# Kernel tuning notes

Hardware: AMD Instinct MI355X
Metric: run time of the kernel (lower is better)

The kernel has to match this reference:

```python
import jax, jax.numpy as jnp
import numpy as np

EPS = 1e-5
NUM_HEADS = 8


def _conv(x, w, pad, dil=1, groups=1, b=None):
    y = jax.lax.conv_general_dilated(
        x, w, (1, 1), pad, rhs_dilation=(dil, dil),
        dimension_numbers=('NCHW', 'OIHW', 'NCHW'), feature_group_count=groups)
    if b is not None:
        y = y + b[None, :, None, None]
    return y


def _bn_relu(x, gamma, beta):
    # BatchNorm2d in training mode: batch statistics over (N,H,W) per channel
    mu = x.mean(axis=(0, 2, 3), keepdims=True)
    var = x.var(axis=(0, 2, 3), keepdims=True)
    y = (x - mu) / jnp.sqrt(var + EPS) * gamma[None, :, None, None] + beta[None, :, None, None]
    return jax.nn.relu(y)


def _ln(x, w, b):
    # WithBias LayerNorm over channel dim (to_3d makes C the last axis)
    mu = x.mean(axis=1, keepdims=True)
    var = x.var(axis=1, keepdims=True)
    return (x - mu) / jnp.sqrt(var + EPS) * w[None, :, None, None] + b[None, :, None, None]


def _l2n(t):
    # torch F.normalize: x / max(||x||_2, 1e-12)
    return t / jnp.maximum(jnp.linalg.norm(t, axis=-1, keepdims=True), 1e-12)


def _forward(x, ln_w, ln_b, wd1, gd1, bd1, wd2, gd2, bd2, wd3, gd3, bd3,
             w_out1, w1, b1, w2, b2, w3, b3, w4, b4, w5, b5, w6, b6, w_out2):
    B, C, H, W = x.shape
    head, ch = NUM_HEADS, C // NUM_HEADS
    x1 = _ln(x, ln_w, ln_b)
    # dilated dense-conv branch (DConv2d = conv -> BN -> ReLU), dilations [1,6,12]
    x11 = _bn_relu(_conv(x, wd1, ((0, 0), (0, 0))), gd1, bd1)
    x12 = _bn_relu(_conv(x, wd2, ((6, 6), (6, 6)), dil=6), gd2, bd2)
    x13 = _bn_relu(_conv(x, wd3, ((12, 12), (12, 12)), dil=12), gd3, bd3)
    out2 = _conv(x11 + x12 + x13, w_out1, ((0, 0), (0, 0))) + x
    # six depthwise conv branches, summed
    att = (_conv(x1, w1, ((0, 0), (2, 2)), groups=C, b=b1)
           + _conv(x1, w2, ((2, 2), (0, 0)), groups=C, b=b2)
           + _conv(x1, w3, ((0, 0), (0, 0)), groups=C, b=b3)
           + _conv(x1, w4, ((1, 1), (1, 1)), groups=C, b=b4)
           + _conv(x1, w5, ((0, 0), (3, 3)), groups=C, b=b5)
           + _conv(x1, w6, ((3, 3), (0, 0)), groups=C, b=b6))
    out1 = _conv(att, w_out2, ((0, 0), (0, 0)))

    def r_hwc(t):  # b (head c) h w -> b head h (w c)
        return t.reshape(B, head, ch, H, W).transpose(0, 1, 3, 4, 2).reshape(B, head, H, W * ch)

    def r_whc(t):  # b (head c) h w -> b head w (h c)
        return t.reshape(B, head, ch, H, W).transpose(0, 1, 4, 3, 2).reshape(B, head, W, H * ch)

    k1 = _l2n(r_hwc(out1))
    v1 = r_hwc(out1)
    k2 = _l2n(r_whc(out2))
    v2 = r_whc(out2)
    q2 = _l2n(r_whc(out1))
    q1 = _l2n(r_whc(out2))
    A1 = jax.nn.softmax(q1 @ jnp.swapaxes(k1, -2, -1), axis=-1)  # [B,head,W,H]
    out3 = A1 @ v1 + q1
    A2 = jax.nn.softmax(q2 @ jnp.swapaxes(k2, -2, -1), axis=-1)
    out4 = A2 @ v2 + q2
    # b head h (w c) -> b (head c) h w
    o3 = out3.reshape(B, head, H, W, ch).transpose(0, 1, 4, 2, 3).reshape(B, C, H, W)
    # b head w (h c) -> b (head c) h w
    o4 = out4.reshape(B, head, W, H, ch).transpose(0, 1, 4, 3, 2).reshape(B, C, H, W)
    return _conv(o3, w_out2, ((0, 0), (0, 0))) + _conv(o4, w_out2, ((0, 0), (0, 0))) + x


def setup_inputs() -> dict:
    key = jax.random.key(0)
    ks = jax.random.split(key, 16)
    B, C, H, W = 8, 128, 128, 128

    def rn(k, shape, s):
        return jax.random.normal(k, shape, jnp.float32) * s

    inp = {}
    inp['x'] = jax.random.normal(ks[0], (B, C, H, W), jnp.float32)
    inp['ln_w'] = jnp.ones((C,), jnp.float32)
    inp['ln_b'] = jnp.zeros((C,), jnp.float32)
    inp['wd1'] = rn(ks[1], (C, C, 1, 1), 0.1)
    inp['gd1'] = jnp.ones((C,), jnp.float32)
    inp['bd1'] = jnp.zeros((C,), jnp.float32)
    inp['wd2'] = rn(ks[2], (C, C, 3, 3), 0.04)
    inp['gd2'] = jnp.ones((C,), jnp.float32)
    inp['bd2'] = jnp.zeros((C,), jnp.float32)
    inp['wd3'] = rn(ks[3], (C, C, 3, 3), 0.04)
    inp['gd3'] = jnp.ones((C,), jnp.float32)
    inp['bd3'] = jnp.zeros((C,), jnp.float32)
    inp['w_out1'] = rn(ks[4], (C, C, 1, 1), 0.09)
    inp['w1'] = rn(ks[5], (C, 1, 1, 5), 0.3)
    inp['b1'] = jnp.zeros((C,), jnp.float32)
    inp['w2'] = rn(ks[6], (C, 1, 5, 1), 0.3)
    inp['b2'] = jnp.zeros((C,), jnp.float32)
    inp['w3'] = rn(ks[7], (C, 1, 1, 1), 0.5)
    inp['b3'] = jnp.zeros((C,), jnp.float32)
    inp['w4'] = rn(ks[8], (C, 1, 3, 3), 0.2)
    inp['b4'] = jnp.zeros((C,), jnp.float32)
    inp['w5'] = rn(ks[9], (C, 1, 1, 7), 0.25)
    inp['b5'] = jnp.zeros((C,), jnp.float32)
    inp['w6'] = rn(ks[10], (C, 1, 7, 1), 0.25)
    inp['b6'] = jnp.zeros((C,), jnp.float32)
    inp['w_out2'] = rn(ks[11], (C, C, 1, 1), 0.09)
    return inp


def reference(x, ln_w, ln_b, wd1, gd1, bd1, wd2, gd2, bd2, wd3, gd3, bd3,
              w_out1, w1, b1, w2, b2, w3, b3, w4, b4, w5, b5, w6, b6, w_out2):
    return _forward(x, ln_w, ln_b, wd1, gd1, bd1, wd2, gd2, bd2, wd3, gd3, bd3,
                    w_out1, w1, b1, w2, b2, w3, b3, w4, b4, w5, b5, w6, b6, w_out2)
```

## Files before the change

kernel.cpp:

```cpp
#include <hip/hip_runtime.h>

#define Bb 8
#define Cc 128
#define Hh 128
#define Ww 128
#define HW 16384
#define CHW (Cc*HW)
#define NHW (Bb*HW)
#define CH 16
#define EPS 1e-5f
#define NSLICE 16

typedef __attribute__((ext_vector_type(8))) short bf16x8;
typedef __attribute__((ext_vector_type(4))) float f32x4;

static __device__ __forceinline__ short f2b(float f) {
  unsigned u = __float_as_uint(f);
  unsigned lsb = (u >> 16) & 1;
  return (short)((u + 0x7fffu + lsb) >> 16);
}
static __device__ __forceinline__ float b2f(short s) {
  return __uint_as_float(((unsigned)(unsigned short)s) << 16);
}

static __device__ __forceinline__ void stats_epilogue(
    float* __restrict__ statp, f32x4 acc[4][4], int co0, int quad, int lm)
{
  statp += (blockIdx.x & (NSLICE-1)) * 768;
  #pragma unroll
  for (int i = 0; i < 4; ++i) {
    f32x4 s = acc[i][0] + acc[i][1] + acc[i][2] + acc[i][3];
    f32x4 q = acc[i][0]*acc[i][0] + acc[i][1]*acc[i][1]
            + acc[i][2]*acc[i][2] + acc[i][3]*acc[i][3];
    #pragma unroll
    for (int m = 1; m < 16; m <<= 1) {
      #pragma unroll
      for (int e = 0; e < 4; ++e) {
        s[e] += __shfl_xor(s[e], m);
        q[e] += __shfl_xor(q[e], m);
      }
    }
    if (lm == 0) {
      int co = co0 + i*16 + quad*4;
      #pragma unroll
      for (int e = 0; e < 4; ++e) {
        atomicAdd(&statp[co + e], s[e]);
        atomicAdd(&statp[128 + co + e], q[e]);
      }
    }
  }
}

__global__ __launch_bounds__(256) void k_ln(const float* __restrict__ x,
    const float* __restrict__ g, const float* __restrict__ be,
    float* __restrict__ y)
{
  int p = blockIdx.x*256 + threadIdx.x;
  int b = p >> 14, hw = p & 16383;
  const float* xp = x + (long)b*CHW + hw;
  float s = 0.f, q = 0.f;
  for (int c = 0; c < Cc; ++c) { float v = xp[c*HW]; s += v; q += v*v; }
  float mu = s * (1.f/Cc);
  float var = q * (1.f/Cc) - mu*mu;
  float rstd = rsqrtf(var + EPS);
  float* yp = y + (long)b*CHW + hw;
  for (int c = 0; c < Cc; ++c) {
    float v = xp[c*HW];
    yp[c*HW] = (v - mu) * rstd * g[c] + be[c];
  }
}

__global__ __launch_bounds__(256) void k_reorg3b(const float* __restrict__ Wt, short* __restrict__ out)
{
  int idx = blockIdx.x*256 + threadIdx.x;
  int tap = idx >> 14, r = idx & 16383;
  out[idx] = f2b(Wt[r*9 + tap]);
}

__global__ __launch_bounds__(256) void k_cast(const float* __restrict__ in, short* __restrict__ out)
{
  int i = blockIdx.x*256 + threadIdx.x;
  out[i] = f2b(in[i]);
}

__global__ __launch_bounds__(256) void k_zero(float* p, int n)
{
  int i = blockIdx.x*256 + threadIdx.x;
  if (i < n) p[i] = 0.f;
}

__global__ __launch_bounds__(256) void k_nhwc(const float* __restrict__ in, short* __restrict__ out)
{
  __shared__ float Ls[32][33];
  int bid = blockIdx.x;
  int hwt = bid & 511, c4 = (bid>>9)&3, b = bid>>11;
  int hw0 = hwt << 5, c0 = c4 << 5;
  int t = threadIdx.x;
  int hl = t & 31, cl = t >> 5;
  const float* p = in + (long)b*CHW + hw0;
  for (int r = cl; r < 32; r += 8)
    Ls[r][hl] = p[(long)(c0+r)*HW + hl];
  __syncthreads();
  short* q = out + ((long)b*HW + hw0)*Cc + c0;
  int ccl = t & 31, hl0 = t >> 5;
  for (int r = hl0; r < 32; r += 8)
    q[(long)r*Cc + ccl] = f2b(Ls[ccl][r]);
}

__global__ __launch_bounds__(256) void k_nhwcb(const short* __restrict__ in, short* __restrict__ out)
{
  __shared__ short Ls[32][34];
  int bid = blockIdx.x;
  int hwt = bid & 511, c4 = (bid>>9)&3, b = bid>>11;
  int hw0 = hwt << 5, c0 = c4 << 5;
  int t = threadIdx.x;
  int hl = t & 31, cl = t >> 5;
  const short* p = in + (long)b*CHW + hw0;
  for (int r = cl; r < 32; r += 8)
    Ls[r][hl] = p[(long)(c0+r)*HW + hl];
  __syncthreads();
  short* q = out + ((long)b*HW + hw0)*Cc + c0;
  int ccl = t & 31, hl0 = t >> 5;
  for (int r = hl0; r < 32; r += 8)
    q[(long)r*Cc + ccl] = Ls[ccl][r];
}

__global__ __launch_bounds__(256,2) void k_mconv(const short* __restrict__ X,
    const short* __restrict__ W, float* __restrict__ Y, int k3, int dil,
    float* __restrict__ statp)
{
  __shared__ short Ws[128*136];
  __shared__ short Xs[152*136];
  int b = blockIdx.x >> 7, h = blockIdx.x & 127;
  int t = threadIdx.x;
  int wave = t >> 6, lane = t & 63;
  int co0 = (wave >> 1) << 6, sp0 = (wave & 1) << 6;
  int lm = lane & 15, quad = lane >> 4;
  f32x4 acc[4][4];
  #pragma unroll
  for (int i = 0; i < 4; ++i)
    #pragma unroll
    for (int j = 0; j < 4; ++j) acc[i][j] = (f32x4){0.f,0.f,0.f,0.f};
  int half = k3 >> 1;

  {
    f32x4 z = {0.f,0.f,0.f,0.f};
    for (int i = t; i < 408; i += 256) {
      int r = i / 17, o = i - r*17;
      int row = r < 12 ? r : r + 128;
      *(f32x4*)(Xs + row*136 + o*8) = z;
    }
  }

  for (int kh = 0; kh < k3; ++kh) {
    int hs = h + (kh - half)*dil;
    if ((unsigned)hs >= (unsigned)Hh) continue;
    __syncthreads();
    {
      const short* xr = X + ((long)(b*Hh + hs)*Ww)*Cc;
      #pragma unroll
      for (int it = 0; it < 8; ++it) {
        int i = t + it*256;
        int row = i >> 4, off = (i & 15) << 3;
        *(f32x4*)(Xs + (12 + row)*136 + off) = *(const f32x4*)(xr + (long)row*Cc + off);
      }
    }
    for (int kw = 0; kw < k3; ++kw) {
      int dw = (kw - half)*dil;
      if (kw) __syncthreads();
      {
        const short* wt = W + (kh*k3 + kw)*16384;
        #pragma unroll
        for (int it = 0; it < 8; ++it) {
          int i = t + it*256;
          int row = i >> 4, off = (i & 15) << 3;
          *(f32x4*)(Ws + row*136 + off) = *(const f32x4*)(wt + (long)row*128 + off);
        }
      }
      __syncthreads();
      int xrow0 = 12 + dw + sp0;
      for (int kc = 0; kc < 4; ++kc) {
        int k0 = kc << 5;
        bf16x8 af[4], bfr[4];
        #pragma unroll
        for (int i = 0; i < 4; ++i)
          af[i] = *(const bf16x8*)(Ws + (co0 + i*16 + lm)*136 + k0 + quad*8);
        #pragma unroll
        for (int j = 0; j < 4; ++j)
          bfr[j] = *(const bf16x8*)(Xs + (xrow0 + j*16 + lm)*136 + k0 + quad*8);
        #pragma unroll
        for (int i = 0; i < 4; ++i)
          #pragma unroll
          for (int j = 0; j < 4; ++j)
            acc[i][j] = __builtin_amdgcn_mfma_f32_16x16x32_bf16(af[i], bfr[j], acc[i][j], 0, 0, 0);
      }
    }
  }
  float* yb = Y + ((long)(b*Hh + h)*Ww)*Cc;
  #pragma unroll
  for (int i = 0; i < 4; ++i) {
    int co = co0 + i*16 + quad*4;
    #pragma unroll
    for (int j = 0; j < 4; ++j) {
      int wc = sp0 + j*16 + lm;
      *(f32x4*)(yb + (long)wc*Cc + co) = acc[i][j];
    }
  }
  if (statp) stats_epilogue(statp, acc, co0, quad, lm);
}

__global__ __launch_bounds__(256,4) void k_mconv1(const short* __restrict__ X,
    const short* __restrict__ W, const float* __restrict__ res,
    float* __restrict__ Y, int nhwc, float* __restrict__ statp)
{
  __shared__ short Ws[128*136];
  int b = blockIdx.x >> 7, h = blockIdx.x & 127;
  int t = threadIdx.x;
  int wave = t >> 6, lane = t & 63;
  int co0 = (wave >> 1) << 6, sp0 = (wave & 1) << 6;
  int lm = lane & 15, quad = lane >> 4;
  #pragma unroll
  for (int it = 0; it < 8; ++it) {
    int i = t + it*256;
    int row = i >> 4, off = (i & 15) << 3;
    *(f32x4*)(Ws + row*136 + off) = *(const f32x4*)(W + (long)row*128 + off);
  }
  f32x4 acc[4][4];
  #pragma unroll
  for (int i = 0; i < 4; ++i)
    #pragma unroll
    for (int j = 0; j < 4; ++j) acc[i][j] = (f32x4){0.f,0.f,0.f,0.f};
  const short* xr = X + ((long)(b*Hh + h)*Ww)*Cc;
  __syncthreads();
  #pragma unroll
  for (int kc = 0; kc < 4; ++kc) {
    int k0 = kc << 5;
    bf16x8 af[4], bfr[4];
    #pragma unroll
    for (int j = 0; j < 4; ++j)
      bfr[j] = *(const bf16x8*)(xr + (long)(sp0 + j*16 + lm)*Cc + k0 + quad*8);
    #pragma unroll
    for (int i = 0; i < 4; ++i)
      af[i] = *(const bf16x8*)(Ws + (co0 + i*16 + lm)*136 + k0 + quad*8);
    #pragma unroll
    for (int i = 0; i < 4; ++i)
      #pragma unroll
      for (int j = 0; j < 4; ++j)
        acc[i][j] = __builtin_amdgcn_mfma_f32_16x16x32_bf16(af[i], bfr[j], acc[i][j], 0, 0, 0);
  }
  if (nhwc) {
    float* yb = Y + ((long)(b*Hh + h)*Ww)*Cc;
    #pragma unroll
    for (int i = 0; i < 4; ++i) {
      int co = co0 + i*16 + quad*4;
      #pragma unroll
      for (int j = 0; j < 4; ++j) {
        int wc = sp0 + j*16 + lm;
        *(f32x4*)(yb + (long)wc*Cc + co) = acc[i][j];
      }
    }
    if (statp) stats_epilogue(statp, acc, co0, quad, lm);
  } else {
    __syncthreads();
    float* scr = (float*)Ws + wave*320;
    int co_l = lane >> 2, wq = (lane & 3) << 2;
    #pragma unroll
    for (int i = 0; i < 4; ++i) {
      #pragma unroll
      for (int j = 0; j < 4; ++j) {
        #pragma unroll
        for (int r = 0; r < 4; ++r)
          scr[(quad*4 + r)*20 + lm] = acc[i][j][r];
        f32x4 vv = *(f32x4*)(scr + co_l*20 + wq);
        int co = co0 + i*16 + co_l;
        int wc = sp0 + j*16 + wq;
        long idx = ((long)(b*Cc + co)*Hh + h)*Ww + wc;
        if (res) vv += *(const f32x4*)(res + idx);
        *(f32x4*)(Y + idx) = vv;
      }
    }
  }
}

__global__ __launch_bounds__(128) void k_bnfin(const float* __restrict__ stats,
    const float* __restrict__ g1, const float* __restrict__ be1,
    const float* __restrict__ g2, const float* __restrict__ be2,
    const float* __restrict__ g3, const float* __restrict__ be3,
    float* __restrict__ so)
{
  int c = threadIdx.x;
  const float inv = 1.f/(float)NHW;
  const float* gs[3] = {g1, g2, g3};
  const float* bs[3] = {be1, be2, be3};
  #pragma unroll
  for (int tsel = 0; tsel < 3; ++tsel) {
    float su = 0.f, qu = 0.f;
    for (int sl = 0; sl < NSLICE; ++sl) {
      su += stats[sl*768 + tsel*256 + c];
      qu += stats[sl*768 + tsel*256 + 128 + c];
    }
    float mu = su*inv;
    float var = qu*inv - mu*mu;
    float s = rsqrtf(var + EPS)*gs[tsel][c];
    so[tsel*256 + c] = s;
    so[tsel*256 + 128 + c] = bs[tsel][c] - mu*s;
  }
}

__global__ __launch_bounds__(256) void k_bnapply(const float* __restrict__ y1,
    const float* __restrict__ y2, const float* __restrict__ y3,
    const float* __restrict__ so, short* __restrict__ sb)
{
  long e = ((long)blockIdx.x*256 + threadIdx.x) * 8;
  int c = (int)(e & 127);
  f32x4 s1a = *(const f32x4*)(so + c),        s1b = *(const f32x4*)(so + c + 4);
  f32x4 o1a = *(const f32x4*)(so + 128 + c),  o1b = *(const f32x4*)(so + 132 + c);
  f32x4 s2a = *(const f32x4*)(so + 256 + c),  s2b = *(const f32x4*)(so + 260 + c);
  f32x4 o2a = *(const f32x4*)(so + 384 + c),  o2b = *(const f32x4*)(so + 388 + c);
  f32x4 s3a = *(const f32x4*)(so + 512 + c),  s3b = *(const f32x4*)(so + 516 + c);
  f32x4 o3a = *(const f32x4*)(so + 640 + c),  o3b = *(const f32x4*)(so + 644 + c);
  f32x4 v1a = *(const f32x4*)(y1 + e), v1b = *(const f32x4*)(y1 + e + 4);
  f32x4 v2a = *(const f32x4*)(y2 + e), v2b = *(const f32x4*)(y2 + e + 4);
  f32x4 v3a = *(const f32x4*)(y3 + e), v3b = *(const f32x4*)(y3 + e + 4);
  float r[8];
  #pragma unroll
  for (int k = 0; k < 4; ++k) {
    r[k] = fmaxf(fmaf(v1a[k], s1a[k], o1a[k]), 0.f)
         + fmaxf(fmaf(v2a[k], s2a[k], o2a[k]), 0.f)
         + fmaxf(fmaf(v3a[k], s3a[k], o3a[k]), 0.f);
    r[4+k] = fmaxf(fmaf(v1b[k], s1b[k], o1b[k]), 0.f)
           + fmaxf(fmaf(v2b[k], s2b[k], o2b[k]), 0.f)
           + fmaxf(fmaf(v3b[k], s3b[k], o3b[k]), 0.f);
  }
  int4 o;
  o.x = ((int)(unsigned short)f2b(r[1])<<16) | (unsigned short)f2b(r[0]);
  o.y = ((int)(unsigned short)f2b(r[3])<<16) | (unsigned short)f2b(r[2]);
  o.z = ((int)(unsigned short)f2b(r[5])<<16) | (unsigned short)f2b(r[4]);
  o.w = ((int)(unsigned short)f2b(r[7])<<16) | (unsigned short)f2b(r[6]);
  *(int4*)(sb + e) = o;
}

__global__ __launch_bounds__(256) void k_dw2(const float* __restrict__ X,
    const float* __restrict__ w1, const float* __restrict__ b1,
    const float* __restrict__ w2, const float* __restrict__ b2,
    const float* __restrict__ w3, const float* __restrict__ b3,
    const float* __restrict__ w4, const float* __restrict__ b4,
    const float* __restrict__ w5, const float* __restrict__ b5,
    const float* __restrict__ w6, const float* __restrict__ b6,
    short* __restrict__ Y)
{
  __shared__ float Ls[38][136];
  int bid = blockIdx.x;
  int tile = bid & 3, plane = bid >> 2;
  int c = plane & 127;
  int h0 = tile << 5;
  int t = threadIdx.x;

  float hcoef[7], vcoef[7], k9[9];
  #pragma unroll
  for (int d = 0; d < 7; ++d) { hcoef[d] = w5[c*7+d]; vcoef[d] = w6[c*7+d]; }
  #pragma unroll
  for (int d = 1; d < 6; ++d) { hcoef[d] += w1[c*5+d-1]; vcoef[d] += w2[c*5+d-1]; }
  hcoef[3] += w3[c];
  #pragma unroll
  for (int k = 0; k < 9; ++k) k9[k] = w4[c*9+k];
  float bias = b1[c]+b2[c]+b3[c]+b4[c]+b5[c]+b6[c];

  const float* xp = X + (long)plane*HW;

  f32x4* lz = (f32x4*)&Ls[0][0];
  for (int i = t; i < 1292; i += 256) lz[i] = (f32x4){0.f,0.f,0.f,0.f};
  __syncthreads();
  for (int i = t; i < 1216; i += 256) {
    int r = i >> 5, cg = (i & 31) << 2;
    int h = h0 - 3 + r;
    if ((unsigned)h < 128u)
      *(f32x4*)&Ls[r][4 + cg] = *(const f32x4*)(xp + h*128 + cg);
  }
  __syncthreads();

  int g = t & 31, rs = t >> 5;
  int w0 = g << 2;
  short* Yp = Y + (long)plane*HW;

  for (int ro = 0; ro < 4; ++ro) {
    int lr = rs + (ro << 3);
    int R = lr + 3;
    f32x4 a0 = *(const f32x4*)&Ls[R][w0];
    f32x4 a1 = *(const f32x4*)&Ls[R][w0+4];
    f32x4 a2 = *(const f32x4*)&Ls[R][w0+8];
    f32x4 u0 = *(const f32x4*)&Ls[R-1][w0];
    f32x4 u1 = *(const f32x4*)&Ls[R-1][w0+4];
    f32x4 u2 = *(const f32x4*)&Ls[R-1][w0+8];
    f32x4 d0 = *(const f32x4*)&Ls[R+1][w0];
    f32x4 d1 = *(const f32x4*)&Ls[R+1][w0+4];
    f32x4 d2 = *(const f32x4*)&Ls[R+1][w0+8];
    f32x4 v3u = *(const f32x4*)&Ls[R-3][w0+4];
    f32x4 v2u = *(const f32x4*)&Ls[R-2][w0+4];
    f32x4 v2d = *(const f32x4*)&Ls[R+2][w0+4];
    f32x4 v3d = *(const f32x4*)&Ls[R+3][w0+4];

    float cr[12], ur[12], dr[12];
    #pragma unroll
    for (int k = 0; k < 4; ++k) {
      cr[k] = a0[k]; cr[4+k] = a1[k]; cr[8+k] = a2[k];
      ur[k] = u0[k]; ur[4+k] = u1[k]; ur[8+k] = u2[k];
      dr[k] = d0[k]; dr[4+k] = d1[k]; dr[8+k] = d2[k];
    }

    float o[4];
    #pragma unroll
    for (int j = 0; j < 4; ++j) {
      float acc = bias;
      #pragma unroll
      for (int d = 0; d < 7; ++d) acc = fmaf(hcoef[d], cr[j+d+1], acc);
      acc = fmaf(vcoef[0], v3u[j], acc);
      acc = fmaf(vcoef[1], v2u[j], acc);
      acc = fmaf(vcoef[2], ur[j+4], acc);
      acc = fmaf(vcoef[3], cr[j+4], acc);
      acc = fmaf(vcoef[4], dr[j+4], acc);
      acc = fmaf(vcoef[5], v2d[j], acc);
      acc = fmaf(vcoef[6], v3d[j], acc);
      #pragma unroll
      for (int kw = 0; kw < 3; ++kw) {
        acc = fmaf(k9[kw],   ur[j+3+kw], acc);
        acc = fmaf(k9[3+kw], cr[j+3+kw], acc);
        acc = fmaf(k9[6+kw], dr[j+3+kw], acc);
      }
      o[j] = acc;
    }
    int2 ov;
    ov.x = ((int)(unsigned short)f2b(o[1])<<16) | (unsigned short)f2b(o[0]);
    ov.y = ((int)(unsigned short)f2b(o[3])<<16) | (unsigned short)f2b(o[2]);
    *(int2*)(Yp + (h0 + lr)*128 + w0) = ov;
  }
}

__global__ __launch_bounds__(256) void k_normh(const float* __restrict__ out1, float* __restrict__ invn)
{
  __shared__ float red[256];
  int bid = blockIdx.x;
  int h = bid & 127; int bh = bid >> 7;
  int b = bh >> 3, hd = bh & 7;
  const float* p = out1 + ((long)(b*Cc + hd*CH)*Hh + h)*Ww;
  float s = 0.f;
  for (int e = threadIdx.x; e < 2048; e += 256) {
    int c = e >> 7, w = e & 127;
    float v = p[(long)c*HW + w];
    s += v*v;
  }
  red[threadIdx.x] = s; __syncthreads();
  for (int st = 128; st > 0; st >>= 1) {
    if (threadIdx.x < st) red[threadIdx.x] += red[threadIdx.x+st];
    __syncthreads();
  }
  if (threadIdx.x == 0) invn[bid] = 1.f/fmaxf(sqrtf(red[0]), 1e-12f);
}

__global__ __launch_bounds__(256) void k_normw_part(const float* __restrict__ out1,
    const float* __restrict__ out2, float* __restrict__ acc1, float* __restrict__ acc2)
{
  __shared__ float red[4][256];
  int bid = blockIdx.x;
  int c = bid & 15, bh = (bid >> 4) & 63, tsel = bid >> 10;
  int b = bh >> 3, hd = bh & 7;
  const float* p = (tsel ? out2 : out1) + (long)(b*Cc + hd*CH + c)*HW;
  int t = threadIdx.x;
  const float4* p4 = (const float4*)p;
  float s0 = 0.f, s1 = 0.f, s2 = 0.f, s3 = 0.f;
  for (int i = t; i < 4096; i += 256) {
    float4 v = p4[i];
    s0 += v.x*v.x; s1 += v.y*v.y; s2 += v.z*v.z; s3 += v.w*v.w;
  }
  red[0][t] = s0; red[1][t] = s1; red[2][t] = s2; red[3][t] = s3;
  __syncthreads();
  if (t < 128) {
    int j = t >> 5;
    int g = t & 31;
    float tot = 0.f;
    #pragma unroll
    for (int r = 0; r < 8; ++r) tot += red[j][g + r*32];
    atomicAdd((tsel ? acc2 : acc1) + bh*128 + g*4 + j, tot);
  }
}

__global__ __launch_bounds__(256) void k_finw(float* __restrict__ p)
{
  int i = blockIdx.x*256 + threadIdx.x;
  float v = p[i];
  p[i] = 1.f/fmaxf(sqrtf(v), 1e-12f);
}

__global__ __launch_bounds__(256) void k_thx(const float* __restrict__ out1,
    const float* __restrict__ out2,
    short* __restrict__ out1T, short* __restrict__ out2T,
    short* __restrict__ out1H, short* __restrict__ out2H)
{
  __shared__ float Ls[32][33];
  int bid = blockIdx.x;
  int wt = bid&3, ht=(bid>>2)&3, c=(bid>>4)&127, b=(bid>>11)&7, src=bid>>14;
  const float* in = (src ? out2 : out1) + (long)(b*128+c)*16384;
  long tbase = ((long)(b*8 + (c>>4))*128)*2048 + (c&15)*128;
  short* pT = (src ? out2T : out1T) + tbase;
  short* pH; long hstr;
  if (src) { pH = out2H + (long)(b*128+c)*16384; hstr = 128; }
  else     { pH = out1H + tbase;                 hstr = 2048; }
  int h0 = ht*32, w0 = wt*32;
  int t = threadIdx.x, li = t&31, r0 = t>>5;
  for (int r = r0; r < 32; r += 8)
    Ls[r][li] = in[(h0+r)*128 + w0 + li];
  __syncthreads();
  for (int r = r0; r < 32; r += 8) {
    pT[(long)(w0+r)*2048 + h0 + li] = f2b(Ls[li][r]);
    pH[(long)(h0+r)*hstr + w0 + li] = f2b(Ls[r][li]);
  }
}

__global__ __launch_bounds__(256) void k_attnS_m(
    const short* __restrict__ out1T, const short* __restrict__ out2T,
    const short* __restrict__ out1H,
    const float* __restrict__ invn1h, const float* __restrict__ invn1w,
    const float* __restrict__ invn2w,
    short* __restrict__ A1b, short* __restrict__ A2b)
{
  __shared__ short As[128*72];
  __shared__ short Bs[128*72];
  int bid = blockIdx.x;
  int type = bid >> 6, bh = bid & 63;
  const short* Aop = (type ? out1T : out2T) + (long)bh*262144;
  const short* Bop = (type ? out2T : out1H) + (long)bh*262144;
  const float* invrow = (type ? invn1w : invn2w) + bh*128;
  const float* invcol = (type ? invn2w : invn1h) + bh*128;
  short* Aout = (type ? A2b : A1b) + (long)bh*16384;
  int t = threadIdx.x;
  int wave = t >> 6, lane = t & 63, lm = lane & 15, quad = lane >> 4;
  int m0 = wave << 5;
  f32x4 acc[2][8];
  #pragma unroll
  for (int i = 0; i < 2; ++i)
    #pragma unroll
    for (int j = 0; j < 8; ++j) acc[i][j] = (f32x4){0.f,0.f,0.f,0.f};
  for (int kc = 0; kc < 32; ++kc) {
    int k0 = kc << 6;
    __syncthreads();
    #pragma unroll
    for (int i = 0; i < 4; ++i) {
      int e = t + i*256;
      int row = e >> 3, off = (e & 7) << 3;
      *(float4*)(As + row*72 + off) = *(const float4*)(Aop + (long)row*2048 + k0 + off);
      *(float4*)(Bs + row*72 + off) = *(const float4*)(Bop + (long)row*2048 + k0 + off);
    }
    __syncthreads();
    #pragma unroll
    for (int ks = 0; ks < 64; ks += 32) {
      bf16x8 af[2], bfj[8];
      #pragma unroll
      for (int i = 0; i < 2; ++i)
        af[i] = *(const bf16x8*)(As + (m0 + i*16 + lm)*72 + ks + quad*8);
      #pragma unroll
      for (int j = 0; j < 8; ++j)
        bfj[j] = *(const bf16x8*)(Bs + (j*16 + lm)*72 + ks + quad*8);
      #pragma unroll
      for (int i = 0; i < 2; ++i)
        #pragma unroll
        for (int j = 0; j < 8; ++j)
          acc[i][j] = __builtin_amdgcn_mfma_f32_16x16x32_bf16(af[i], bfj[j], acc[i][j], 0, 0, 0);
    }
  }
  float colv[8];
  #pragma unroll
  for (int j = 0; j < 8; ++j) colv[j] = invcol[j*16 + lm];
  #pragma unroll
  for (int i = 0; i < 2; ++i) {
    #pragma unroll
    for (int r = 0; r < 4; ++r) {
      int row = m0 + i*16 + quad*4 + r;
      float rs = invrow[row];
      float sv[8];
      float mx = -1e30f;
      #pragma unroll
      for (int j = 0; j < 8; ++j) {
        sv[j] = acc[i][j][r] * rs * colv[j];
        mx = fmaxf(mx, sv[j]);
      }
      mx = fmaxf(mx, __shfl_xor(mx, 1));
      mx = fmaxf(mx, __shfl_xor(mx, 2));
      mx = fmaxf(mx, __shfl_xor(mx, 4));
      mx = fmaxf(mx, __shfl_xor(mx, 8));
      float sum = 0.f;
      #pragma unroll
      for (int j = 0; j < 8; ++j) { sv[j] = __expf(sv[j] - mx); sum += sv[j]; }
      sum += __shfl_xor(sum, 1);
      sum += __shfl_xor(sum, 2);
      sum += __shfl_xor(sum, 4);
      sum += __shfl_xor(sum, 8);
      float inv = 1.f/sum;
      #pragma unroll
      for (int j = 0; j < 8; ++j)
        Aout[row*128 + j*16 + lm] = f2b(sv[j]*inv);
    }
  }
}

__global__ __launch_bounds__(256) void k_o34f(
    const short* __restrict__ A1b, const short* __restrict__ out1T,
    const short* __restrict__ out1H, const float* __restrict__ invn1w,
    const short* __restrict__ out2H, const short* __restrict__ A2b,
    const float* __restrict__ out2, const float* __restrict__ invn2w,
    short* __restrict__ o34b)
{
  __shared__ short As[128*72];
  __shared__ short Bs[128*72];
  int bid = blockIdx.x;
  int cf = bid & 127, b = bid >> 7;
  int hd = cf >> 4, c = cf & 15;
  int bh = b*8 + hd;
  const short* A0 = A1b + (long)bh*16384;
  const short* B0 = out1T + (long)bh*262144 + c*128;
  const short* A1_ = out2H + (long)(b*128 + cf)*16384;
  const short* B1_ = A2b + (long)bh*16384;
  const short* R = out1H + (long)bh*262144 + c*128;
  const float* o2p = out2 + (long)(b*128 + cf)*16384;
  const float* inw1 = invn1w + bh*128;
  const float* inw2 = invn2w + bh*128;
  short* O = o34b + (long)(b*128 + cf)*16384;
  int t = threadIdx.x;
  int wave = t >> 6, lane = t & 63, lm = lane & 15, quad = lane >> 4;
  int m0 = (wave >> 1) << 6, n0 = (wave & 1) << 6;
  f32x4 acc[4][4];
  #pragma unroll
  for (int i = 0; i < 4; ++i)
    #pragma unroll
    for (int j = 0; j < 4; ++j) acc[i][j] = (f32x4){0.f,0.f,0.f,0.f};
  for (int g = 0; g < 4; ++g) {
    const short* Asrc = (g < 2) ? A0 : A1_;
    const short* Bsrc = (g < 2) ? B0 : B1_;
    long Bst = (g < 2) ? 2048 : 128;
    int k0 = (g & 1) << 6;
    __syncthreads();
    #pragma unroll
    for (int i = 0; i < 4; ++i) {
      int e = t + i*256;
      int row = e >> 3, off = (e & 7) << 3;
      *(float4*)(As + row*72 + off) = *(const float4*)(Asrc + (long)row*128 + k0 + off);
      *(float4*)(Bs + row*72 + off) = *(const float4*)(Bsrc + (long)row*Bst + k0 + off);
    }
    __syncthreads();
    #pragma unroll
    for (int ks = 0; ks < 64; ks += 32) {
      bf16x8 af[4], bfj[4];
      #pragma unroll
      for (int i = 0; i < 4; ++i)
        af[i] = *(const bf16x8*)(As + (m0 + i*16 + lm)*72 + ks + quad*8);
      #pragma unroll
      for (int j = 0; j < 4; ++j)
        bfj[j] = *(const bf16x8*)(Bs + (n0 + j*16 + lm)*72 + ks + quad*8);
      #pragma unroll
      for (int i = 0; i < 4; ++i)
        #pragma unroll
        for (int j = 0; j < 4; ++j)
          acc[i][j] = __builtin_amdgcn_mfma_f32_16x16x32_bf16(af[i], bfj[j], acc[i][j], 0, 0, 0);
    }
  }
  float inwv[4];
  #pragma unroll
  for (int j = 0; j < 4; ++j) inwv[j] = inw1[n0 + j*16 + lm];
  #pragma unroll
  for (int i = 0; i < 4; ++i) {
    int row0 = m0 + i*16 + quad*4;
    f32x4 iv2 = *(const f32x4*)(inw2 + row0);
    #pragma unroll
    for (int j = 0; j < 4; ++j) {
      int col = n0 + j*16 + lm;
      f32x4 vq = *(const f32x4*)(o2p + (long)col*128 + row0);
      #pragma unroll
      for (int r = 0; r < 4; ++r)
        acc[i][j][r] += b2f(R[(long)(row0 + r)*2048 + col]) * inwv[j]
                      + vq[r] * iv2[r];
    }
  }
  __syncthreads();
  float* scr = (float*)As + wave*320;
  int co_l = lane >> 2, wq = (lane & 3) << 2;
  #pragma unroll
  for (int i = 0; i < 4; ++i) {
    #pragma unroll
    for (int j = 0; j < 4; ++j) {
      #pragma unroll
      for (int r = 0; r < 4; ++r)
        scr[(quad*4 + r)*20 + lm] = acc[i][j][r];
      f32x4 vv = *(f32x4*)(scr + co_l*20 + wq);
      int2 ov;
      ov.x = ((int)(unsigned short)f2b(vv[1])<<16) | (unsigned short)f2b(vv[0]);
      ov.y = ((int)(unsigned short)f2b(vv[3])<<16) | (unsigned short)f2b(vv[2]);
      *(int2*)(O + (long)(m0 + i*16 + co_l)*128 + n0 + j*16 + wq) = ov;
    }
  }
}

extern "C" void kernel_launch(void* const* d_in, const int* in_sizes, int n_in,
                              void* d_out, int out_size, void* d_ws, size_t ws_size,
                              hipStream_t stream)
{
  const float* x    = (const float*)d_in[0];
  const float* ln_w = (const float*)d_in[1];
  const float* ln_b = (const float*)d_in[2];
  const float* wd1  = (const float*)d_in[3];
  const float* gd1  = (const float*)d_in[4];
  const float* bd1  = (const float*)d_in[5];
  const float* wd2  = (const float*)d_in[6];
  const float* gd2  = (const float*)d_in[7];
  const float* bd2  = (const float*)d_in[8];
  const float* wd3  = (const float*)d_in[9];
  const float* gd3  = (const float*)d_in[10];
  const float* bd3  = (const float*)d_in[11];
  const float* w_out1 = (const float*)d_in[12];
  const float* w1 = (const float*)d_in[13]; const float* b1 = (const float*)d_in[14];
  const float* w2 = (const float*)d_in[15]; const float* b2 = (const float*)d_in[16];
  const float* w3 = (const float*)d_in[17]; const float* b3 = (const float*)d_in[18];
  const float* w4 = (const float*)d_in[19]; const float* b4 = (const float*)d_in[20];
  const float* w5 = (const float*)d_in[21]; const float* b5 = (const float*)d_in[22];
  const float* w6 = (const float*)d_in[23]; const float* b6 = (const float*)d_in[24];
  const float* w_out2 = (const float*)d_in[25];
  float* out = (float*)d_out;

  const long SLAB = 16777216L;
  float* buf0 = (float*)d_ws;
  float* buf1 = buf0 + SLAB;
  float* buf2 = buf1 + SLAB;
  float* dbuf = out;
  float* stats = buf2 + SLAB;
  float* invn1h = stats + NSLICE*768;
  float* invn1w = invn1h + 8192;
  float* invn2w = invn1w + 8192;
  short* wb2  = (short*)(invn2w + 8192);
  short* wb3  = wb2 + 147456;
  short* wb1  = wb3 + 147456;
  short* wbo1 = wb1 + 16384;
  short* wbo2 = wbo1 + 16384;
  short* A1b  = wbo2 + 16384;
  short* A2b  = A1b + 1048576;
  float* bnso = (float*)(A2b + 1048576);

  short* xb = (short*)buf0;
  short* sb = (short*)buf0;
  short* attb = (short*)dbuf;
  short* ab = (short*)buf1;
  short* out1T = (short*)dbuf;
  short* out2T = out1T + 16777216;
  short* out1H = (short*)buf1;
  short* out2H = out1H + 16777216;
  short* o34b = (short*)buf0;
  short* ob = (short*)buf1;

  k_zero<<<48, 256, 0, stream>>>(stats, NSLICE*768);
  k_zero<<<64, 256, 0, stream>>>(invn1w, 16384);
  k_reorg3b<<<576, 256, 0, stream>>>(wd2, wb2);
  k_reorg3b<<<576, 256, 0, stream>>>(wd3, wb3);
  k_cast<<<64, 256, 0, stream>>>(wd1, wb1);
  k_cast<<<64, 256, 0, stream>>>(w_out1, wbo1);
  k_cast<<<64, 256, 0, stream>>>(w_out2, wbo2);

  k_nhwc<<<16384, 256, 0, stream>>>(x, xb);
  k_mconv1<<<1024, 256, 0, stream>>>(xb, wb1, nullptr, buf1, 1, stats);
  k_mconv<<<1024, 256, 0, stream>>>(xb, wb2, buf2, 3, 6, stats + 256);
  k_mconv<<<1024, 256, 0, stream>>>(xb, wb3, dbuf, 3, 12, stats + 512);
  k_bnfin<<<1, 128, 0, stream>>>(stats, gd1, bd1, gd2, bd2, gd3, bd3, bnso);
  k_bnapply<<<8192, 256, 0, stream>>>(buf1, buf2, dbuf, bnso, sb);
  k_mconv1<<<1024, 256, 0, stream>>>(sb, wbo1, x, buf2, 0, nullptr);
  k_ln<<<512, 256, 0, stream>>>(x, ln_w, ln_b, buf0);
  k_dw2<<<4096, 256, 0, stream>>>(buf0, w1,b1,w2,b2,w3,b3,w4,b4,w5,b5,w6,b6, attb);
  k_nhwcb<<<16384, 256, 0, stream>>>(attb, ab);
  k_mconv1<<<1024, 256, 0, stream>>>(ab, wbo2, nullptr, buf0, 0, nullptr);
  k_normh<<<8192, 256, 0, stream>>>(buf0, invn1h);
  k_normw_part<<<2048, 256, 0, stream>>>(buf0, buf2, invn1w, invn2w);
  k_finw<<<64, 256, 0, stream>>>(invn1w);
  k_thx<<<32768, 256, 0, stream>>>(buf0, buf2, out1T, out2T, out1H, out2H);
  k_attnS_m<<<128, 256, 0, stream>>>(out1T, out2T, out1H,
                                     invn1h, invn1w, invn2w, A1b, A2b);
  k_o34f<<<1024, 256, 0, stream>>>(A1b, out1T, out1H, invn1w,
                                   out2H, A2b, buf2, invn2w, o34b);
  k_nhwcb<<<16384, 256, 0, stream>>>(o34b, ob);
  k_mconv1<<<1024, 256, 0, stream>>>(ob, wbo2, x, out, 0, nullptr);
}
```

Before: 758.8 us.

## Fuse L2-norm reductions into transpose kernel and split attention-score rows across blocks

Removes the separate k_normh and k_normw_part passes by computing the per-row and per-column squared sums from the shared-memory tile inside k_thx, accumulated with atomics, so out1/out2 are not re-read for normalisation. A single k_finw then converts all three norm buffers. Separately, k_attnS_m splits each 128-row score matrix into two 64-row halves, doubling the grid from 128 to 256 blocks for better occupancy at the cost of loading the B operand twice. This relies on invn1h, invn1w and invn2w being contiguous, and it adds many atomics to k_thx.

Result: no change. 765.3 us (+0.9%).

```diff
diff --git a/kernel.cpp b/kernel.cpp
--- a/kernel.cpp
+++ b/kernel.cpp
@@ -436,54 +436,6 @@
   }
 }
 
-__global__ __launch_bounds__(256) void k_normh(const float* __restrict__ out1, float* __restrict__ invn)
-{
-  __shared__ float red[256];
-  int bid = blockIdx.x;
-  int h = bid & 127; int bh = bid >> 7;
-  int b = bh >> 3, hd = bh & 7;
-  const float* p = out1 + ((long)(b*Cc + hd*CH)*Hh + h)*Ww;
-  float s = 0.f;
-  for (int e = threadIdx.x; e < 2048; e += 256) {
-    int c = e >> 7, w = e & 127;
-    float v = p[(long)c*HW + w];
-    s += v*v;
-  }
-  red[threadIdx.x] = s; __syncthreads();
-  for (int st = 128; st > 0; st >>= 1) {
-    if (threadIdx.x < st) red[threadIdx.x] += red[threadIdx.x+st];
-    __syncthreads();
-  }
-  if (threadIdx.x == 0) invn[bid] = 1.f/fmaxf(sqrtf(red[0]), 1e-12f);
-}
-
-__global__ __launch_bounds__(256) void k_normw_part(const float* __restrict__ out1,
-    const float* __restrict__ out2, float* __restrict__ acc1, float* __restrict__ acc2)
-{
-  __shared__ float red[4][256];
-  int bid = blockIdx.x;
-  int c = bid & 15, bh = (bid >> 4) & 63, tsel = bid >> 10;
-  int b = bh >> 3, hd = bh & 7;
-  const float* p = (tsel ? out2 : out1) + (long)(b*Cc + hd*CH + c)*HW;
-  int t = threadIdx.x;
-  const float4* p4 = (const float4*)p;
-  float s0 = 0.f, s1 = 0.f, s2 = 0.f, s3 = 0.f;
-  for (int i = t; i < 4096; i += 256) {
-    float4 v = p4[i];
-    s0 += v.x*v.x; s1 += v.y*v.y; s2 += v.z*v.z; s3 += v.w*v.w;
-  }
-  red[0][t] = s0; red[1][t] = s1; red[2][t] = s2; red[3][t] = s3;
-  __syncthreads();
-  if (t < 128) {
-    int j = t >> 5;
-    int g = t & 31;
-    float tot = 0.f;
-    #pragma unroll
-    for (int r = 0; r < 8; ++r) tot += red[j][g + r*32];
-    atomicAdd((tsel ? acc2 : acc1) + bh*128 + g*4 + j, tot);
-  }
-}
-
 __global__ __launch_bounds__(256) void k_finw(float* __restrict__ p)
 {
   int i = blockIdx.x*256 + threadIdx.x;
@@ -494,7 +446,8 @@
 __global__ __launch_bounds__(256) void k_thx(const float* __restrict__ out1,
     const float* __restrict__ out2,
     short* __restrict__ out1T, short* __restrict__ out2T,
-    short* __restrict__ out1H, short* __restrict__ out2H)
+    short* __restrict__ out1H, short* __restrict__ out2H,
+    float* __restrict__ n1h, float* __restrict__ n1w, float* __restrict__ n2w)
 {
   __shared__ float Ls[32][33];
   int bid = blockIdx.x;
@@ -510,6 +463,19 @@
   for (int r = r0; r < 32; r += 8)
     Ls[r][li] = in[(h0+r)*128 + w0 + li];
   __syncthreads();
+  int bhbase = (b*8 + (c>>4))*128;
+  if (t < 32) {
+    if (!src) {
+      float s = 0.f;
+      for (int k = 0; k < 32; ++k) { float v = Ls[t][k]; s += v*v; }
+      atomicAdd(&n1h[bhbase + h0 + t], s);
+    }
+  } else if (t < 64) {
+    int w = t - 32;
+    float s = 0.f;
+    for (int k = 0; k < 32; ++k) { float v = Ls[k][w]; s += v*v; }
+    atomicAdd((src ? n2w : n1w) + bhbase + w0 + w, s);
+  }
   for (int r = r0; r < 32; r += 8) {
     pT[(long)(w0+r)*2048 + h0 + li] = f2b(Ls[li][r]);
     pH[(long)(h0+r)*hstr + w0 + li] = f2b(Ls[r][li]);
@@ -523,82 +489,78 @@
     const float* __restrict__ invn2w,
     short* __restrict__ A1b, short* __restrict__ A2b)
 {
-  __shared__ short As[128*72];
+  __shared__ short As[64*72];
   __shared__ short Bs[128*72];
   int bid = blockIdx.x;
-  int type = bid >> 6, bh = bid & 63;
-  const short* Aop = (type ? out1T : out2T) + (long)bh*262144;
+  int rh = bid & 1, bh = (bid >> 1) & 63, type = bid >> 7;
+  const short* Aop = (type ? out1T : out2T) + (long)bh*262144 + (long)rh*131072;
   const short* Bop = (type ? out2T : out1H) + (long)bh*262144;
-  const float* invrow = (type ? invn1w : invn2w) + bh*128;
+  const float* invrow = (type ? invn1w : invn2w) + bh*128 + rh*64;
   const float* invcol = (type ? invn2w : invn1h) + bh*128;
-  short* Aout = (type ? A2b : A1b) + (long)bh*16384;
+  short* Aout = (type ? A2b : A1b) + (long)bh*16384 + rh*8192;
   int t = threadIdx.x;
   int wave = t >> 6, lane = t & 63, lm = lane & 15, quad = lane >> 4;
-  int m0 = wave << 5;
-  f32x4 acc[2][8];
-  #pragma unroll
-  for (int i = 0; i < 2; ++i)
-    #pragma unroll
-    for (int j = 0; j < 8; ++j) acc[i][j] = (f32x4){0.f,0.f,0.f,0.f};
+  int m0 = wave << 4;
+  f32x4 acc[8];
+  #pragma unroll
+  for (int j = 0; j < 8; ++j) acc[j] = (f32x4){0.f,0.f,0.f,0.f};
   for (int kc = 0; kc < 32; ++kc) {
     int k0 = kc << 6;
     __syncthreads();
     #pragma unroll
+    for (int i = 0; i < 2; ++i) {
+      int e = t + i*256;
+      int row = e >> 3, off = (e & 7) << 3;
+      *(float4*)(As + row*72 + off) = *(const float4*)(Aop + (long)row*2048 + k0 + off);
+    }
+    #pragma unroll
     for (int i = 0; i < 4; ++i) {
       int e = t + i*256;
       int row = e >> 3, off = (e & 7) << 3;
-      *(float4*)(As + row*72 + off) = *(const float4*)(Aop + (long)row*2048 + k0 + off);
       *(float4*)(Bs + row*72 + off) = *(const float4*)(Bop + (long)row*2048 + k0 + off);
     }
     __syncthreads();
     #pragma unroll
     for (int ks = 0; ks < 64; ks += 32) {
-      bf16x8 af[2], bfj[8];
-      #pragma unroll
-      for (int i = 0; i < 2; ++i)
-        af[i] = *(const bf16x8*)(As + (m0 + i*16 + lm)*72 + ks + quad*8);
+      bf16x8 af, bfj[8];
+      af = *(const bf16x8*)(As + (m0 + lm)*72 + ks + quad*8);
       #pragma unroll
       for (int j = 0; j < 8; ++j)
         bfj[j] = *(const bf16x8*)(Bs + (j*16 + lm)*72 + ks + quad*8);
       #pragma unroll
-      for (int i = 0; i < 2; ++i)
-        #pragma unroll
-        for (int j = 0; j < 8; ++j)
-          acc[i][j] = __builtin_amdgcn_mfma_f32_16x16x32_bf16(af[i], bfj[j], acc[i][j], 0, 0, 0);
+      for (int j = 0; j < 8; ++j)
+        acc[j] = __builtin_amdgcn_mfma_f32_16x16x32_bf16(af, bfj[j], acc[j], 0, 0, 0);
     }
   }
   float colv[8];
   #pragma unroll
   for (int j = 0; j < 8; ++j) colv[j] = invcol[j*16 + lm];
   #pragma unroll
-  for (int i = 0; i < 2; ++i) {
-    #pragma unroll
-    for (int r = 0; r < 4; ++r) {
-      int row = m0 + i*16 + quad*4 + r;
-      float rs = invrow[row];
-      float sv[8];
-      float mx = -1e30f;
-      #pragma unroll
-      for (int j = 0; j < 8; ++j) {
-        sv[j] = acc[i][j][r] * rs * colv[j];
-        mx = fmaxf(mx, sv[j]);
-      }
-      mx = fmaxf(mx, __shfl_xor(mx, 1));
-      mx = fmaxf(mx, __shfl_xor(mx, 2));
-      mx = fmaxf(mx, __shfl_xor(mx, 4));
-      mx = fmaxf(mx, __shfl_xor(mx, 8));
-      float sum = 0.f;
-      #pragma unroll
-      for (int j = 0; j < 8; ++j) { sv[j] = __expf(sv[j] - mx); sum += sv[j]; }
-      sum += __shfl_xor(sum, 1);
-      sum += __shfl_xor(sum, 2);
-      sum += __shfl_xor(sum, 4);
-      sum += __shfl_xor(sum, 8);
-      float inv = 1.f/sum;
-      #pragma unroll
-      for (int j = 0; j < 8; ++j)
-        Aout[row*128 + j*16 + lm] = f2b(sv[j]*inv);
-    }
+  for (int r = 0; r < 4; ++r) {
+    int row = m0 + quad*4 + r;
+    float rs = invrow[row];
+    float sv[8];
+    float mx = -1e30f;
+    #pragma unroll
+    for (int j = 0; j < 8; ++j) {
+      sv[j] = acc[j][r] * rs * colv[j];
+      mx = fmaxf(mx, sv[j]);
+    }
+    mx = fmaxf(mx, __shfl_xor(mx, 1));
+    mx = fmaxf(mx, __shfl_xor(mx, 2));
+    mx = fmaxf(mx, __shfl_xor(mx, 4));
+    mx = fmaxf(mx, __shfl_xor(mx, 8));
+    float sum = 0.f;
+    #pragma unroll
+    for (int j = 0; j < 8; ++j) { sv[j] = __expf(sv[j] - mx); sum += sv[j]; }
+    sum += __shfl_xor(sum, 1);
+    sum += __shfl_xor(sum, 2);
+    sum += __shfl_xor(sum, 4);
+    sum += __shfl_xor(sum, 8);
+    float inv = 1.f/sum;
+    #pragma unroll
+    for (int j = 0; j < 8; ++j)
+      Aout[row*128 + j*16 + lm] = f2b(sv[j]*inv);
   }
 }
 
@@ -754,7 +716,7 @@
   short* ob = (short*)buf1;
 
   k_zero<<<48, 256, 0, stream>>>(stats, NSLICE*768);
-  k_zero<<<64, 256, 0, stream>>>(invn1w, 16384);
+  k_zero<<<96, 256, 0, stream>>>(invn1h, 24576);
   k_reorg3b<<<576, 256, 0, stream>>>(wd2, wb2);
   k_reorg3b<<<576, 256, 0, stream>>>(wd3, wb3);
   k_cast<<<64, 256, 0, stream>>>(wd1, wb1);
@@ -772,11 +734,10 @@
   k_dw2<<<4096, 256, 0, stream>>>(buf0, w1,b1,w2,b2,w3,b3,w4,b4,w5,b5,w6,b6, attb);
   k_nhwcb<<<16384, 256, 0, stream>>>(attb, ab);
   k_mconv1<<<1024, 256, 0, stream>>>(ab, wbo2, nullptr, buf0, 0, nullptr);
-  k_normh<<<8192, 256, 0, stream>>>(buf0, invn1h);
-  k_normw_part<<<2048, 256, 0, stream>>>(buf0, buf2, invn1w, invn2w);
-  k_finw<<<64, 256, 0, stream>>>(invn1w);
-  k_thx<<<32768, 256, 0, stream>>>(buf0, buf2, out1T, out2T, out1H, out2H);
-  k_attnS_m<<<128, 256, 0, stream>>>(out1T, out2T, out1H,
+  k_thx<<<32768, 256, 0, stream>>>(buf0, buf2, out1T, out2T, out1H, out2H,
+                                   invn1h, invn1w, invn2w);
+  k_finw<<<96, 256, 0, stream>>>(invn1h);
+  k_attnS_m<<<256, 256, 0, stream>>>(out1T, out2T, out1H,
                                      invn1h, invn1w, invn2w, A1b, A2b);
   k_o34f<<<1024, 256, 0, stream>>>(A1b, out1T, out1H, invn1w,
                                    out2H, A2b, buf2, invn2w, o34b);
```
